# Kernel tuning notes

Measured on AMD Instinct MI355X. Metric: run time of the kernel, lower is better.

The kernel has to match this reference:

```python
import jax, jax.numpy as jnp
import numpy as np

BETA = 0.25  # commitment loss weight (standard VQ-VAE)


def setup_inputs() -> dict:
    key = jax.random.key(0)
    k1, k2, k3, k4 = jax.random.split(key, 4)
    B, C, H, W, K = 4, 4, 64, 64, 8192
    return {
        "z": jax.random.normal(k1, (B, C, H, W), dtype=jnp.float32),
        "pre_quant_w": jax.random.normal(k2, (C, C), dtype=jnp.float32) * 0.1,
        "pre_quant_b": jax.random.normal(k3, (C,), dtype=jnp.float32) * 0.1,
        "codebook": jax.random.normal(k4, (K, C), dtype=jnp.float32),
    }


def reference(z, pre_quant_w, pre_quant_b, codebook):
    B, C, H, W = z.shape
    # 1x1 pre-quant conv (kernel [out_c, in_c])
    zq = jnp.einsum('bchw,oc->bohw', z, pre_quant_w) + pre_quant_b[None, :, None, None]
    # to [B, N, C] token layout (matches permute(0,2,3,1).reshape)
    x = zq.transpose(0, 2, 3, 1).reshape(B, H * W, C)
    # squared euclidean distance to every codebook entry: [B, N, K]
    d = (jnp.sum(x * x, axis=-1, keepdims=True)
         - 2.0 * jnp.einsum('bnc,kc->bnk', x, codebook)
         + jnp.sum(codebook * codebook, axis=-1)[None, None, :])
    idx = jnp.argmin(d, axis=-1)               # [B, N] nearest codebook index
    quant = codebook[idx]                      # gather: [B, N, C]
    commitment_loss = jnp.mean((jax.lax.stop_gradient(quant) - x) ** 2)
    codebook_loss = jnp.mean((quant - jax.lax.stop_gradient(x)) ** 2)
    loss = codebook_loss + BETA * commitment_loss
    # straight-through estimator
    quant_st = x + jax.lax.stop_gradient(quant - x)
    quant_st = quant_st.reshape(B, H, W, C).transpose(0, 3, 1, 2)  # [B, C, H, W]
    return quant_st, loss
```

## Files before the change

### kernel.cpp

```cpp
#include <hip/hip_runtime.h>

static constexpr int TOKENS = 16384;
static constexpr int HW     = 4096;
static constexpr int NSG    = 64;
static constexpr int ESG    = 128;
static constexpr int NGROUP = 16;
static constexpr int GTOK   = 1024;
static constexpr int TPT    = 4;

__global__ __launch_bounds__(256) void k_init(
    unsigned long long* __restrict__ A, float* __restrict__ acc,
    unsigned* __restrict__ cnt)
{
    int i = blockIdx.x * 256 + threadIdx.x;
    A[i] = 0xFFFFFFFFFFFFFFFFull;
    if (i == 0) { *acc = 0.0f; *cnt = 0u; }
}

__global__ __launch_bounds__(256, 4) void k_dist(
    const float* __restrict__ z,
    const float* __restrict__ w,
    const float* __restrict__ bias,
    const float4* __restrict__ CB,
    unsigned long long* __restrict__ A)
{
    const int bx  = blockIdx.x;
    const int g   = bx & (NGROUP - 1);
    const int s   = bx >> 4;
    const int tid = threadIdx.x;

    const int tbase = g * GTOK + tid;
    float m0[TPT], m1[TPT], m2[TPT], m3[TPT], bv[TPT], x2s[TPT];
    int bi[TPT];
#pragma unroll
    for (int j = 0; j < TPT; ++j) {
        int t = tbase + j * 256;
        int b = t >> 12;
        int n = t & (HW - 1);
        const float* zb = z + b * (4 * HW) + n;
        float z0 = zb[0], z1 = zb[HW], z2 = zb[2 * HW], z3 = zb[3 * HW];
        float x0 = fmaf(w[3],  z3, fmaf(w[2],  z2, fmaf(w[1],  z1, fmaf(w[0],  z0, bias[0]))));
        float x1 = fmaf(w[7],  z3, fmaf(w[6],  z2, fmaf(w[5],  z1, fmaf(w[4],  z0, bias[1]))));
        float x2 = fmaf(w[11], z3, fmaf(w[10], z2, fmaf(w[9],  z1, fmaf(w[8],  z0, bias[2]))));
        float x3 = fmaf(w[15], z3, fmaf(w[14], z2, fmaf(w[13], z1, fmaf(w[12], z0, bias[3]))));
        m0[j] = -2.0f * x0;
        m1[j] = -2.0f * x1;
        m2[j] = -2.0f * x2;
        m3[j] = -2.0f * x3;
        x2s[j] = fmaf(x3, x3, fmaf(x2, x2, fmaf(x1, x1, x0 * x0)));
        bv[j] = 3.0e38f;
        bi[j] = 0;
    }

    const int sbase = __builtin_amdgcn_readfirstlane(s * ESG);
    const float4* __restrict__ cs = CB + sbase;

#pragma unroll 8
    for (int e = 0; e < ESG; ++e) {
        float4 c = cs[e];
        float cn = fmaf(c.w, c.w, fmaf(c.z, c.z, fmaf(c.y, c.y, c.x * c.x)));
#pragma unroll
        for (int j = 0; j < TPT; ++j) {
            float d = fmaf(m0[j], c.x, fmaf(m1[j], c.y, fmaf(m2[j], c.z, fmaf(m3[j], c.w, cn))));
            bool lt = d < bv[j];
            bv[j] = lt ? d : bv[j];
            bi[j] = lt ? e : bi[j];
        }
    }

#pragma unroll
    for (int j = 0; j < TPT; ++j) {
        float D = bv[j] + x2s[j];
        unsigned u = __float_as_uint(D);
        u ^= (unsigned)((int)u >> 31) | 0x80000000u;
        unsigned long long key =
            ((unsigned long long)u << 32) | (unsigned)(sbase + bi[j]);
        atomicMin(&A[tbase + j * 256], key);
    }
}

__global__ __launch_bounds__(256) void k_out(
    const float* __restrict__ z,
    const float* __restrict__ w,
    const float* __restrict__ bias,
    const float4* __restrict__ CB,
    const unsigned long long* __restrict__ A,
    float* __restrict__ out,
    float* __restrict__ acc,
    unsigned* __restrict__ cnt)
{
    int t = blockIdx.x * 256 + threadIdx.x;
    int b = t >> 12;
    int n = t & (HW - 1);

    const float* zb = z + b * (4 * HW) + n;
    float z0 = zb[0], z1 = zb[HW], z2 = zb[2 * HW], z3 = zb[3 * HW];
    float x0 = fmaf(w[3],  z3, fmaf(w[2],  z2, fmaf(w[1],  z1, fmaf(w[0],  z0, bias[0]))));
    float x1 = fmaf(w[7],  z3, fmaf(w[6],  z2, fmaf(w[5],  z1, fmaf(w[4],  z0, bias[1]))));
    float x2 = fmaf(w[11], z3, fmaf(w[10], z2, fmaf(w[9],  z1, fmaf(w[8],  z0, bias[2]))));
    float x3 = fmaf(w[15], z3, fmaf(w[14], z2, fmaf(w[13], z1, fmaf(w[12], z0, bias[3]))));

    int idx = (int)((unsigned)A[t] & 8191u);
    float4 qv = CB[idx];
    float d0 = qv.x - x0, d1 = qv.y - x1, d2 = qv.z - x2, d3 = qv.w - x3;

    float* ob = out + b * (4 * HW) + n;
    ob[0]      = x0 + d0;
    ob[HW]     = x1 + d1;
    ob[2 * HW] = x2 + d2;
    ob[3 * HW] = x3 + d3;

    float ls = fmaf(d3, d3, fmaf(d2, d2, fmaf(d1, d1, d0 * d0)));
#pragma unroll
    for (int off = 32; off > 0; off >>= 1)
        ls += __shfl_down(ls, off, 64);
    __shared__ float wsum[4];
    if ((threadIdx.x & 63) == 0) wsum[threadIdx.x >> 6] = ls;
    __syncthreads();
    if (threadIdx.x == 0) {
        atomicAdd(acc, wsum[0] + wsum[1] + wsum[2] + wsum[3]);
        __threadfence();
        unsigned old = atomicAdd(cnt, 1u);
        if (old == gridDim.x - 1) {
            float m = atomicAdd(acc, 0.0f) * (1.0f / 65536.0f);
            out[TOKENS * 4] = m + 0.25f * m;
        }
    }
}

extern "C" void kernel_launch(void* const* d_in, const int* in_sizes, int n_in,
                              void* d_out, int out_size, void* d_ws, size_t ws_size,
                              hipStream_t stream)
{
    const float* z    = (const float*)d_in[0];
    const float* w    = (const float*)d_in[1];
    const float* bias = (const float*)d_in[2];
    const float* cb   = (const float*)d_in[3];
    float* out = (float*)d_out;

    char* ws = (char*)d_ws;
    float*              acc = (float*)ws;
    unsigned*           cnt = (unsigned*)(ws + 256);
    unsigned long long* A   = (unsigned long long*)(ws + 1024);

    const float4* CB4 = (const float4*)cb;

    k_init<<<TOKENS / 256, 256, 0, stream>>>(A, acc, cnt);
    k_dist<<<NSG * NGROUP, 256, 0, stream>>>(z, w, bias, CB4, A);
    k_out<<<TOKENS / 256, 256, 0, stream>>>(z, w, bias, CB4, A, out, acc, cnt);
}
```

Before: 39.55 us.

## Fuse output/loss epilogue into distance kernel via per-group last-block counter

Folds the separate output kernel into the distance kernel. Each token group gets an atomic counter, and the last of its 64 codebook-slice blocks to finish reads the final atomicMin keys, gathers the codewords, writes the straight-through output and adds to the loss. This removes one kernel launch and the recomputation of the pre-quant conv. In exchange, the epilogue runs on only 16 blocks, each handling 4 tokens per thread, and the kernel now relies on threadfence and atomic ordering across blocks.

```diff
diff --git a/kernel.cpp b/kernel.cpp
--- a/kernel.cpp
+++ b/kernel.cpp
@@ -9,20 +9,27 @@
 static constexpr int TPT    = 4;
 
 __global__ __launch_bounds__(256) void k_init(
-    unsigned long long* __restrict__ A, float* __restrict__ acc,
-    unsigned* __restrict__ cnt)
+    unsigned long long* __restrict__ A,
+    float* __restrict__ acc, unsigned* __restrict__ done,
+    unsigned* __restrict__ gcnt)
 {
     int i = blockIdx.x * 256 + threadIdx.x;
     A[i] = 0xFFFFFFFFFFFFFFFFull;
-    if (i == 0) { *acc = 0.0f; *cnt = 0u; }
+    if (blockIdx.x == 0) {
+        if (threadIdx.x < NGROUP) gcnt[threadIdx.x] = 0u;
+        if (threadIdx.x == NGROUP) { *acc = 0.0f; *done = 0u; }
+    }
 }
 
-__global__ __launch_bounds__(256, 4) void k_dist(
+__global__ __launch_bounds__(256, 4) void k_fused(
     const float* __restrict__ z,
     const float* __restrict__ w,
     const float* __restrict__ bias,
     const float4* __restrict__ CB,
-    unsigned long long* __restrict__ A)
+    unsigned long long* __restrict__ A,
+    float* __restrict__ out,
+    float* __restrict__ acc, unsigned* __restrict__ done,
+    unsigned* __restrict__ gcnt)
 {
     const int bx  = blockIdx.x;
     const int g   = bx & (NGROUP - 1);
@@ -54,7 +61,6 @@
 
     const int sbase = __builtin_amdgcn_readfirstlane(s * ESG);
     const float4* __restrict__ cs = CB + sbase;
-
 #pragma unroll 8
     for (int e = 0; e < ESG; ++e) {
         float4 c = cs[e];
@@ -77,51 +83,45 @@
             ((unsigned long long)u << 32) | (unsigned)(sbase + bi[j]);
         atomicMin(&A[tbase + j * 256], key);
     }
-}
 
-__global__ __launch_bounds__(256) void k_out(
-    const float* __restrict__ z,
-    const float* __restrict__ w,
-    const float* __restrict__ bias,
-    const float4* __restrict__ CB,
-    const unsigned long long* __restrict__ A,
-    float* __restrict__ out,
-    float* __restrict__ acc,
-    unsigned* __restrict__ cnt)
-{
-    int t = blockIdx.x * 256 + threadIdx.x;
-    int b = t >> 12;
-    int n = t & (HW - 1);
+    __threadfence();
+    __shared__ int lastflag;
+    if (tid == 0) lastflag = (atomicAdd(&gcnt[g], 1u) == NSG - 1);
+    __syncthreads();
+    if (!lastflag) return;
 
-    const float* zb = z + b * (4 * HW) + n;
-    float z0 = zb[0], z1 = zb[HW], z2 = zb[2 * HW], z3 = zb[3 * HW];
-    float x0 = fmaf(w[3],  z3, fmaf(w[2],  z2, fmaf(w[1],  z1, fmaf(w[0],  z0, bias[0]))));
-    float x1 = fmaf(w[7],  z3, fmaf(w[6],  z2, fmaf(w[5],  z1, fmaf(w[4],  z0, bias[1]))));
-    float x2 = fmaf(w[11], z3, fmaf(w[10], z2, fmaf(w[9],  z1, fmaf(w[8],  z0, bias[2]))));
-    float x3 = fmaf(w[15], z3, fmaf(w[14], z2, fmaf(w[13], z1, fmaf(w[12], z0, bias[3]))));
+    float ls = 0.0f;
+#pragma unroll
+    for (int j = 0; j < TPT; ++j) {
+        int t = tbase + j * 256;
+        unsigned long long key = atomicAdd(&A[t], 0ull);
+        int idx = (int)(key & 8191u);
+        float4 qv = CB[idx];
+        float x0 = -0.5f * m0[j];
+        float x1 = -0.5f * m1[j];
+        float x2 = -0.5f * m2[j];
+        float x3 = -0.5f * m3[j];
+        float d0 = qv.x - x0, d1 = qv.y - x1, d2 = qv.z - x2, d3 = qv.w - x3;
+        int b = t >> 12;
+        int n = t & (HW - 1);
+        float* ob = out + b * (4 * HW) + n;
+        ob[0]      = x0 + d0;
+        ob[HW]     = x1 + d1;
+        ob[2 * HW] = x2 + d2;
+        ob[3 * HW] = x3 + d3;
+        ls += fmaf(d3, d3, fmaf(d2, d2, fmaf(d1, d1, d0 * d0)));
+    }
 
-    int idx = (int)((unsigned)A[t] & 8191u);
-    float4 qv = CB[idx];
-    float d0 = qv.x - x0, d1 = qv.y - x1, d2 = qv.z - x2, d3 = qv.w - x3;
-
-    float* ob = out + b * (4 * HW) + n;
-    ob[0]      = x0 + d0;
-    ob[HW]     = x1 + d1;
-    ob[2 * HW] = x2 + d2;
-    ob[3 * HW] = x3 + d3;
-
-    float ls = fmaf(d3, d3, fmaf(d2, d2, fmaf(d1, d1, d0 * d0)));
 #pragma unroll
     for (int off = 32; off > 0; off >>= 1)
         ls += __shfl_down(ls, off, 64);
     __shared__ float wsum[4];
-    if ((threadIdx.x & 63) == 0) wsum[threadIdx.x >> 6] = ls;
+    if ((tid & 63) == 0) wsum[tid >> 6] = ls;
     __syncthreads();
-    if (threadIdx.x == 0) {
+    if (tid == 0) {
         atomicAdd(acc, wsum[0] + wsum[1] + wsum[2] + wsum[3]);
         __threadfence();
-        unsigned old = atomicAdd(cnt, 1u);
-        if (old == gridDim.x - 1) {
+        if (atomicAdd(done, 1u) == NGROUP - 1) {
             float m = atomicAdd(acc, 0.0f) * (1.0f / 65536.0f);
             out[TOKENS * 4] = m + 0.25f * m;
         }
@@ -139,13 +139,13 @@
     float* out = (float*)d_out;
 
     char* ws = (char*)d_ws;
-    float*              acc = (float*)ws;
-    unsigned*           cnt = (unsigned*)(ws + 256);
-    unsigned long long* A   = (unsigned long long*)(ws + 1024);
+    float*              acc  = (float*)ws;
+    unsigned*           done = (unsigned*)(ws + 64);
+    unsigned*           gcnt = (unsigned*)(ws + 128);
+    unsigned long long* A    = (unsigned long long*)(ws + 1024);
 
     const float4* CB4 = (const float4*)cb;
 
-    k_init<<<TOKENS / 256, 256, 0, stream>>>(A, acc, cnt);
-    k_dist<<<NSG * NGROUP, 256, 0, stream>>>(z, w, bias, CB4, A);
-    k_out<<<TOKENS / 256, 256, 0, stream>>>(z, w, bias, CB4, A, out, acc, cnt);
+    k_init<<<TOKENS / 256, 256, 0, stream>>>(A, acc, done, gcnt);
+    k_fused<<<NSG * NGROUP, 256, 0, stream>>>(z, w, bias, CB4, A, out, acc, done, gcnt);
 }
```

Result: slower. 82.51 us (+108.6%).
